# Performance work log

Measured on AMD Instinct MI355X. Metric: run time of the kernel, lower is better.

## Reference

```python
import jax, jax.numpy as jnp
import numpy as np

FS = 44100
LS = 1323000  # 30 s at 44.1 kHz (Ls/fs = 30 exactly)
FMIN, FMAX, BNDS = 32.7, 20000.0, 96
MIN_WIN = 4


def _design():
    """Reimplementation of LogScale + nsgfwin(sliced=False) + calcwinrange +
    the matrixform nsgtf loop parameters, producing a dense gather-index
    matrix idx [nbins, Mmax] and window matrix gw [nbins, Mmax]."""
    odiv = (np.log2(FMAX) - np.log2(FMIN)) / (BNDS - 1)
    pow2n = 2.0 ** odiv
    f = FMIN * pow2n ** np.arange(BNDS)
    lbas = BNDS
    frqs = np.concatenate(([0.0], f, [FS / 2.0]))
    fbas = np.concatenate((frqs, FS - frqs[-2:0:-1]))  # mirror negative freqs
    fbas *= float(LS) / FS
    # bandwidths M (window lengths)
    M = np.zeros(len(fbas), dtype=np.int64)
    M[0] = np.round(2 * fbas[1])
    for k in range(1, 2 * lbas + 1):
        M[k] = np.round(fbas[k + 1] - fbas[k - 1])
    M[-1] = np.round(LS - fbas[-2])
    M = np.maximum(M, MIN_WIN)
    # Hann windows (zero-frequency centered, hannwin)
    g = [0.5 * (np.cos(np.arange(m) * (2.0 * np.pi / m)) + 1.0) for m in M]
    # center positions rfbas (calcwinrange -> timepos == rfbas, nn == Ls)
    fb = fbas.copy()
    fb[lbas] = (fbas[lbas - 1] + fbas[lbas + 1]) / 2
    fb[lbas + 2] = LS - fb[lbas]
    rfbas = np.round(fb).astype(np.int64)
    nbins = len(g) // 2 + 1        # real=True, reducedform=0
    Mmax = int(M[:nbins].max())    # matrixform: all bins padded to Mmax
    idx = np.zeros((nbins, Mmax), dtype=np.int32)
    gw = np.zeros((nbins, Mmax), dtype=np.float32)
    for j in range(nbins):
        gj = g[j]
        Lg = len(gj)
        win = (np.arange(-(Lg // 2), Lg - (Lg // 2)) + rfbas[j]) % LS
        gs = np.fft.fftshift(gj)  # g is real -> conj is a no-op
        h1, h2 = (Lg + 1) // 2, Lg // 2
        # nsgtf placement: temp[:h1] = t[h2:], temp[-h2:] = t[:h2]
        idx[j, :h1] = win[h2:]
        gw[j, :h1] = gs[h2:]
        if h2 > 0:
            idx[j, Mmax - h2:] = win[:h2]
            gw[j, Mmax - h2:] = gs[:h2]
    return idx, gw


def setup_inputs() -> dict:
    key = jax.random.key(0)
    idx, gw = _design()
    s = jax.random.normal(key, (2, LS), dtype=jnp.float32)  # [channels, Ls]
    return {"s": s, "idx": jnp.asarray(idx), "gw": jnp.asarray(gw)}


def reference(s, idx, gw):
    # NSGT forward (nsgtf, matrixform, real): FFT the signal, gather each
    # frequency bin's circular window range, multiply by the fftshifted
    # window, zero-pad into a length-Mmax buffer, and IFFT per bin.
    ft = jnp.fft.fft(s.astype(jnp.complex64))          # [B, Ls]
    t = ft[:, idx] * gw                                # [B, nbins, Mmax]
    c = jnp.fft.ifft(t, axis=-1)                       # complex coefficients
    # pack complex output as trailing (real, imag) float32 channel
    return jnp.stack((c.real, c.imag), axis=-1)        # [B, nbins, Mmax, 2]
```

## Files before the change

### kernel.cpp

```cpp
#include <hip/hip_runtime.h>

#define LS 1323000
#define NB 98
#define MM 123000
#define N2 3000
#define BATCH 2
#define NROWS_T (NB*BATCH)
#define TWO_PI 6.28318530717958647692f

#define KBN 188
#define QN  96
#define SROW (KBN*QN*16)
#define QP  104

#define TBL2_OFF 0
#define TBL3_OFF 20
#define TBL4_OFF 120
#define TBL5_OFF 370
#define TBL_N    2995

typedef __attribute__((ext_vector_type(8))) short short8;
typedef __attribute__((ext_vector_type(4))) float f32x4;

__device__ __forceinline__ float2 cmul(float2 a, float2 b){
  return make_float2(a.x*b.x - a.y*b.y, a.x*b.y + a.y*b.x);
}
__device__ __forceinline__ unsigned short f2bf(float f){
  unsigned int u = __float_as_uint(f);
  unsigned int r = (u + 0x7FFFu + ((u >> 16) & 1u)) >> 16;
  return (unsigned short)r;
}

template<int R,int S>
__device__ __forceinline__ void butterfly(float2* v){
  if constexpr (R==4){
    float2 t0=make_float2(v[0].x+v[2].x, v[0].y+v[2].y);
    float2 t1=make_float2(v[0].x-v[2].x, v[0].y-v[2].y);
    float2 t2=make_float2(v[1].x+v[3].x, v[1].y+v[3].y);
    float2 t3=make_float2(v[1].x-v[3].x, v[1].y-v[3].y);
    v[0]=make_float2(t0.x+t2.x, t0.y+t2.y);
    v[2]=make_float2(t0.x-t2.x, t0.y-t2.y);
    v[1]=make_float2(t1.x - (float)S*t3.y, t1.y + (float)S*t3.x);
    v[3]=make_float2(t1.x + (float)S*t3.y, t1.y - (float)S*t3.x);
  } else if constexpr (R==8){
    float2 e[4]={v[0],v[2],v[4],v[6]};
    float2 o[4]={v[1],v[3],v[5],v[7]};
    butterfly<4,S>(e);
    butterfly<4,S>(o);
    const float h = 0.70710678118654752440f;
    float2 w1=make_float2(h, (float)S*h);
    float2 w2=make_float2(0.f, (float)S);
    float2 w3=make_float2(-h, (float)S*h);
    float2 o1=cmul(o[1],w1), o2=cmul(o[2],w2), o3=cmul(o[3],w3);
    v[0]=make_float2(e[0].x+o[0].x, e[0].y+o[0].y);
    v[4]=make_float2(e[0].x-o[0].x, e[0].y-o[0].y);
    v[1]=make_float2(e[1].x+o1.x, e[1].y+o1.y);
    v[5]=make_float2(e[1].x-o1.x, e[1].y-o1.y);
    v[2]=make_float2(e[2].x+o2.x, e[2].y+o2.y);
    v[6]=make_float2(e[2].x-o2.x, e[2].y-o2.y);
    v[3]=make_float2(e[3].x+o3.x, e[3].y+o3.y);
    v[7]=make_float2(e[3].x-o3.x, e[3].y-o3.y);
  } else {
    float2 x[R];
    #pragma unroll
    for(int k=0;k<R;k++){
      float2 acc=v[0];
      #pragma unroll
      for(int n=1;n<R;n++){
        const int p=(k*n)%R;
        float ang = (float)S * (TWO_PI/(float)R) * (float)p;
        float sn,cs; __sincosf(ang,&sn,&cs);
        acc.x += v[n].x*cs - v[n].y*sn;
        acc.y += v[n].x*sn + v[n].y*cs;
      }
      x[k]=acc;
    }
    #pragma unroll
    for(int k=0;k<R;k++) v[k]=x[k];
  }
}

template<int R,int S>
__global__ void __launch_bounds__(256)
fft_pass(const float2* __restrict__ in, float2* __restrict__ out,
         int N, int Ns){
  const int T = N / R;
  int j = blockIdx.x*blockDim.x + threadIdx.x;
  if (j >= T) return;
  int t = j % Ns;
  float u = (float)t / (float)(Ns*R);
  float ang = (float)S * TWO_PI * u;
  float sn,cs; __sincosf(ang,&sn,&cs);
  float2 w1=make_float2(cs,sn);
  float2 wr=make_float2(1.f,0.f);
  float2 v[R];
  #pragma unroll
  for(int r=0;r<R;r++){
    float2 a = in[j + r*T];
    v[r] = cmul(a, wr);
    wr = cmul(wr, w1);
  }
  butterfly<R,S>(v);
  int d = (j/Ns)*(Ns*R) + t;
  #pragma unroll
  for(int r=0;r<R;r++) out[d + r*Ns] = v[r];
}

__global__ void __launch_bounds__(256)
fft_c2c8(const float* __restrict__ s, float2* __restrict__ y){
  const int T = LS/8;
  int j = blockIdx.x*blockDim.x + threadIdx.x;
  if (j >= T) return;
  const float* x0 = s;
  const float* x1 = s + LS;
  float2 v[8];
  #pragma unroll
  for(int r=0;r<8;r++) v[r] = make_float2(x0[j + r*T], x1[j + r*T]);
  butterfly<8,-1>(v);
  int d = 8*j;
  #pragma unroll
  for(int r=0;r<8;r++) y[d + r] = v[r];
}

__global__ void span_init(int* __restrict__ spanA, int* __restrict__ spanB){
  int j = blockIdx.x*blockDim.x + threadIdx.x;
  if (j < NB){ spanA[j] = 0; spanB[j] = MM; }
}

#define SPAN_SLICE 4096
__global__ void __launch_bounds__(256)
rowspan_par(const float* __restrict__ gw, int* __restrict__ spanA,
            int* __restrict__ spanB){
  const int j  = blockIdx.x;
  const int lo = blockIdx.y * SPAN_SLICE;
  const int end = min(lo + SPAN_SLICE, MM);
  const float* g = gw + (size_t)j*MM;
  const int tid = threadIdx.x;
  int mA = -1, mB = MM;
  for (int m = lo + tid*4; m < end; m += 256*4){
    float4 v = *(const float4*)(g + m);
    #pragma unroll
    for (int t = 0; t < 4; t++){
      float f = ((const float*)&v)[t];
      int m2 = m + t;
      if (f != 0.f){
        if (m2 < 61500){ if (m2 > mA) mA = m2; }
        else           { if (m2 < mB) mB = m2; }
      }
    }
  }
  __shared__ int sA[256], sB[256];
  sA[tid]=mA; sB[tid]=mB; __syncthreads();
  for (int s=128; s>0; s>>=1){
    if (tid<s){ sA[tid]=max(sA[tid],sA[tid+s]); sB[tid]=min(sB[tid],sB[tid+s]); }
    __syncthreads();
  }
  if (tid==0){
    if (sA[0] >= 0) atomicMax(&spanA[j], sA[0]+1);
    if (sB[0] < MM) atomicMin(&spanB[j], sB[0]);
  }
}

__global__ void __launch_bounds__(256)
a_prep(unsigned short* __restrict__ A96){
  int i = blockIdx.x*blockDim.x + threadIdx.x;
  if (i >= 96*QP) return;
  int R = i / QP, q = i - R*QP;
  float val = 0.f;
  if (R < 82 && q < 82){
    int k2 = R >> 1, c = R & 1, n2 = q >> 1, cp = q & 1;
    int p = (k2*n2) % 41;
    float ang = (float)p * (TWO_PI/41.f);
    float sn, cs; sincosf(ang, &sn, &cs);
    val = c ? (cp ? cs : sn) : (cp ? -sn : cs);
  }
  A96[i] = f2bf(val);
}

__global__ void __launch_bounds__(256)
twid_prep(float2* __restrict__ tbl){
  int i = blockIdx.x*blockDim.x + threadIdx.x;
  if (i >= TBL_N) return;
  int t, r, den;
  if (i < TBL3_OFF)      { int l=i;          t=l/4; r=l%4+1; den=25;   }
  else if (i < TBL4_OFF) { int l=i-TBL3_OFF; t=l/4; r=l%4+1; den=125;  }
  else if (i < TBL5_OFF) { int l=i-TBL4_OFF; t=l/2; r=l%2+1; den=375;  }
  else                   { int l=i-TBL5_OFF; t=l/7; r=l%7+1; den=3000; }
  float ang = TWO_PI * (float)(t*r) / (float)den;
  float sn, cs; sincosf(ang, &sn, &cs);
  tbl[i] = make_float2(cs, sn);
}

#define PTILE 1681
__global__ void __launch_bounds__(256)
pack_gather(const float2* __restrict__ ft, const int* __restrict__ idx,
            const float* __restrict__ gw, const int* __restrict__ spanA,
            const int* __restrict__ spanB, float2* __restrict__ T, int row0){
  const int row  = row0 + blockIdx.y;
  const int jrow = row % NB;
  const int b    = row / NB;
  const int spA = spanA[jrow], spB = spanB[jrow];
  const int base = blockIdx.x * PTILE;
  const int end  = min(base + PTILE, MM);
  if (!(base < spA || end > spB)) return;
  __shared__ float2 tile[PTILE];
  const int cnt = end - base;
  const int*   idxr = idx + (size_t)jrow*MM;
  const float* gwr  = gw  + (size_t)jrow*MM;
  for (int l = threadIdx.x; l < cnt; l += 256){
    int n = base + l;
    float g = gwr[n] * (1.0f/(float)MM);
    int id = idxr[n];
    float2 F1 = ft[id];
    float2 F2 = ft[id ? (LS - id) : 0];
    float2 f;
    if (b == 0) f = make_float2(0.5f*(F1.x + F2.x), 0.5f*(F1.y - F2.y));
    else        f = make_float2(0.5f*(F1.y + F2.y), 0.5f*(F2.x - F1.x));
    tile[l] = make_float2(f.x*g, f.y*g);
  }
  __syncthreads();
  float2* Trow = T + (size_t)blockIdx.y*MM;
  const int bm = base % 41;
  for (int l2 = threadIdx.x; l2 < PTILE; l2 += 256){
    int n2 = l2 / 41, w = l2 - 41*n2;
    int l0 = n2 - bm; if (l0 < 0) l0 += 41;
    int l = l0 + 41*w;
    if (l < cnt){
      int n = base + l;
      if (n < spA || n >= spB){
        int ig = n / 41;
        Trow[(size_t)n2*N2 + ig] = tile[l];
      }
    }
  }
}

template<int R>
__device__ __forceinline__ void lds_stage1(const float2* src, float2* dst, int tid){
  const int T = N2 / R;
  for (int j = tid; j < T; j += 256){
    float2 v[R];
    #pragma unroll
    for (int r = 0; r < R; r++) v[r] = src[j + r*T];
    butterfly<R,1>(v);
    int d = j*R;
    #pragma unroll
    for (int r = 0; r < R; r++) dst[d + r] = v[r];
  }
}

template<int R, int Ns>
__device__ __forceinline__ void lds_stage_t(const float2* src, float2* dst,
                                            int tid, const float2* tw){
  const int T = N2 / R;
  for (int j = tid; j < T; j += 256){
    int t = j % Ns;
    const float2* w = tw + t*(R-1);
    float2 v[R];
    v[0] = src[j];
    #pragma unroll
    for (int r = 1; r < R; r++) v[r] = cmul(src[j + r*T], w[r-1]);
    butterfly<R,1>(v);
    int d = (j/Ns)*(Ns*R) + t;
    #pragma unroll
    for (int r = 0; r < R; r++) dst[d + r*Ns] = v[r];
  }
}

__global__ void __launch_bounds__(256)
inv_s1(const float2* __restrict__ T, const int* __restrict__ spanA,
       const int* __restrict__ spanB, const float2* __restrict__ tbl,
       unsigned short* __restrict__ Bb, int row0){
  __shared__ float2 u0[N2];
  __shared__ float2 u1[N2];
  __shared__ float2 tlds[TBL5_OFF];
  const int n2  = blockIdx.x;
  const int jrow = (row0 + blockIdx.y) % NB;
  const int tid = threadIdx.x;
  const int spA = spanA[jrow], spB = spanB[jrow];
  const int n1A = (spA - n2 + 40) / 41;
  const int n1B = (spB - n2 + 40) / 41;
  const float2* Trow = T + (size_t)blockIdx.y*MM + (size_t)n2*N2;
  for (int i = tid; i < N2; i += 256){
    float2 val = make_float2(0.f, 0.f);
    if (i < n1A || i >= n1B) val = Trow[i];
    u0[i] = val;
  }
  for (int i = tid; i < TBL5_OFF; i += 256) tlds[i] = tbl[i];
  __syncthreads();
  lds_stage1<5>(u0, u1, tid);                          __syncthreads();
  lds_stage_t<5,5>  (u1, u0, tid, tlds + TBL2_OFF);    __syncthreads();
  lds_stage_t<5,25> (u0, u1, tid, tlds + TBL3_OFF);    __syncthreads();
  lds_stage_t<3,125>(u1, u0, tid, tlds + TBL4_OFF);    __syncthreads();

  unsigned short* Brow = Bb + (size_t)blockIdx.y*SROW;
  const float2* tbl5 = tbl + TBL5_OFF;
  const int qr = 2*n2, qi = 2*n2+1;
  float sn, cs;
  __sincosf((float)(n2*375) * (TWO_PI/(float)MM), &sn, &cs);
  const float2 wstep = make_float2(cs, sn);
  for (int j = tid; j < 375; j += 256){
    const float2* w = tbl5 + j*7;
    float2 v[8];
    v[0] = u0[j];
    #pragma unroll
    for (int r = 1; r < 8; r++) v[r] = cmul(u0[j + r*375], w[r-1]);
    butterfly<8,1>(v);
    float ang = (float)(n2*j) * (TWO_PI/(float)MM);
    __sincosf(ang, &sn, &cs);
    float2 wf = make_float2(cs, sn);
    #pragma unroll
    for (int r = 0; r < 8; r++){
      float2 o = cmul(v[r], wf);
      int k1 = j + 375*r;
      int kb = k1 >> 4, kl = k1 & 15;
      size_t base = (size_t)kb*(QN*16) + kl;
      Brow[base + qr*16] = f2bf(o.x);
      Brow[base + qi*16] = f2bf(o.y);
      wf = cmul(wf, wstep);
    }
  }
}

__global__ void __launch_bounds__(256)
inv_s2_mfma(const unsigned short* __restrict__ A96,
            const unsigned short* __restrict__ Bb,
            float2* __restrict__ out){
  __shared__ unsigned short Als[96*QP];
  __shared__ unsigned short Bls[64*QP];
  const int tid = threadIdx.x;

  {
    const uint4* src = (const uint4*)A96;
    uint4* dst = (uint4*)Als;
    for (int f = tid; f < (96*QP*2)/16; f += 256) dst[f] = src[f];
  }
  {
    const unsigned short* Bt = Bb + (size_t)blockIdx.y*SROW
                                  + (size_t)blockIdx.x*4*(QN*16);
    for (int f = tid; f < 768; f += 256){
      uint4 d = *(const uint4*)(Bt + (size_t)f*8);
      int q   = (f >> 1) % QN;
      int kb  = f / (QN*2);
      int kl0 = (f & 1) * 8;
      if (q >= 82) d = make_uint4(0u,0u,0u,0u);
      const unsigned short* e = (const unsigned short*)&d;
      int rbase = kb*16 + kl0;
      #pragma unroll
      for (int j = 0; j < 8; j++)
        Bls[(rbase + j)*QP + q] = e[j];
    }
  }
  __syncthreads();

  const int w = tid >> 6, l = tid & 63;
  const int g = l >> 4, c = l & 15;

  f32x4 acc[6];
  #pragma unroll
  for (int m = 0; m < 6; m++) acc[m] = (f32x4){0.f,0.f,0.f,0.f};

  short8 b0 = *(const short8*)&Bls[(16*w + c)*QP +  0 + 8*g];
  short8 b1 = *(const short8*)&Bls[(16*w + c)*QP + 32 + 8*g];
  short8 b2 = *(const short8*)&Bls[(16*w + c)*QP + 64 + 8*g];
  #pragma unroll
  for (int m = 0; m < 6; m++){
    short8 a0 = *(const short8*)&Als[(16*m + c)*QP +  0 + 8*g];
    short8 a1 = *(const short8*)&Als[(16*m + c)*QP + 32 + 8*g];
    short8 a2 = *(const short8*)&Als[(16*m + c)*QP + 64 + 8*g];
    acc[m] = __builtin_amdgcn_mfma_f32_16x16x32_bf16(a0, b0, acc[m], 0, 0, 0);
    acc[m] = __builtin_amdgcn_mfma_f32_16x16x32_bf16(a1, b1, acc[m], 0, 0, 0);
    acc[m] = __builtin_amdgcn_mfma_f32_16x16x32_bf16(a2, b2, acc[m], 0, 0, 0);
  }

  float2* orow = out + (size_t)blockIdx.y*MM;
  int k1 = blockIdx.x*64 + 16*w + c;
  if (k1 < N2){
    #pragma unroll
    for (int m = 0; m < 6; m++){
      int R0 = 16*m + 4*g;
      int k2a = R0 >> 1;
      int k2b = k2a + 1;
      if (k2a < 41) orow[(size_t)k2a*N2 + k1] = make_float2(acc[m][0], acc[m][1]);
      if (k2b < 41) orow[(size_t)k2b*N2 + k1] = make_float2(acc[m][2], acc[m][3]);
    }
  }
}

extern "C" void kernel_launch(void* const* d_in, const int* in_sizes, int n_in,
                              void* d_out, int out_size, void* d_ws, size_t ws_size,
                              hipStream_t stream){
  const float* s   = (const float*)d_in[0];
  const int*   idx = (const int*)d_in[1];
  const float* gw  = (const float*)d_in[2];
  float2* out = (float2*)d_out;
  char* ws = (char*)d_ws;

  const size_t FWD_BYTES = 10584064;
  float2* bufA = (float2*)ws;
  float2* bufB = (float2*)(ws + FWD_BYTES);
  int* spanA = (int*)(ws + 2*FWD_BYTES);
  int* spanB = (int*)(ws + 2*FWD_BYTES + 512);
  unsigned short* A96 = (unsigned short*)(ws + 2*FWD_BYTES + 1024);
  const size_t A_BYTES = 20480;
  float2* tbl = (float2*)(ws + 2*FWD_BYTES + 1024 + A_BYTES);
  const size_t TBL_BYTES = 24576;
  unsigned short* Bbase = (unsigned short*)(ws + 2*FWD_BYTES + 1024 + A_BYTES + TBL_BYTES);

  a_prep<<<(96*QP + 255)/256, 256, 0, stream>>>(A96);
  twid_prep<<<(TBL_N + 255)/256, 256, 0, stream>>>(tbl);
  span_init<<<1, 128, 0, stream>>>(spanA, spanB);
  {
    dim3 g(NB, (MM + SPAN_SLICE - 1)/SPAN_SLICE);
    rowspan_par<<<g, 256, 0, stream>>>(gw, spanA, spanB);
  }

  {
    int blks = (LS/8 + 255)/256;
    fft_c2c8<<<blks,256,0,stream>>>(s, bufA);
  }
  float2* cur = bufA; float2* nxt = bufB;
  int Ns = 8;
  #define FWD(R) do{                                                         \
    int blks = (LS/(R) + 255)/256;                                           \
    fft_pass<R,-1><<<blks,256,0,stream>>>(cur, nxt, LS, Ns);                 \
    Ns *= (R);                                                               \
    { float2* tmp=cur; cur=nxt; nxt=tmp; }                                   \
  }while(0)
  FWD(7); FWD(7); FWD(5); FWD(5); FWD(5); FWD(3); FWD(3); FWD(3);
  #undef FWD

  const size_t row_bytes = (size_t)SROW * 2;
  size_t used = 2*FWD_BYTES + 1024 + A_BYTES + TBL_BYTES;
  size_t avail = (ws_size > used) ? (ws_size - used) : 0;
  int max_chunk = (int)(avail / row_bytes);
  if (max_chunk > NROWS_T) max_chunk = NROWS_T;
  if (max_chunk < 1) max_chunk = 1;

  const int ptiles = (MM + PTILE - 1)/PTILE;
  for (int c0 = 0; c0 < NROWS_T; c0 += max_chunk){
    int cr = NROWS_T - c0; if (cr > max_chunk) cr = max_chunk;
    float2* Tchunk = out + (size_t)c0*MM;
    dim3 g0(ptiles, cr);
    pack_gather<<<g0,256,0,stream>>>(cur, idx, gw, spanA, spanB, Tchunk, c0);
    dim3 g1(41, cr);
    inv_s1<<<g1,256,0,stream>>>(Tchunk, spanA, spanB, tbl, Bbase, c0);
    dim3 g2(47, cr);
    inv_s2_mfma<<<g2,256,0,stream>>>(A96, Bbase, Tchunk);
  }
}
```

Before: 515.0 us.

## Use radix-15 forward FFT passes and widen inverse stage-one blocks

Replaces the six radix-5/radix-3 forward FFT passes with three radix-15 passes built from a 3x5 prime-factor butterfly. This cuts the number of full-signal global memory round trips in the forward transform. Also raises the inv_s1 block size to 512 threads and pads the twiddle tables to 5/3 strides. The cost is more registers per radix-15 thread and different occupancy in inv_s1.

```diff
diff --git a/kernel.cpp b/kernel.cpp
--- a/kernel.cpp
+++ b/kernel.cpp
@@ -13,11 +13,13 @@
 #define SROW (KBN*QN*16)
 #define QP  104
 
-#define TBL2_OFF 0
-#define TBL3_OFF 20
-#define TBL4_OFF 120
-#define TBL5_OFF 370
-#define TBL_N    2995
+#define P2 0
+#define P3 25
+#define P4 150
+#define P5 525
+#define TBL_N 3150
+
+#define NT1 512
 
 typedef __attribute__((ext_vector_type(8))) short short8;
 typedef __attribute__((ext_vector_type(4))) float f32x4;
@@ -60,6 +62,39 @@
     v[6]=make_float2(e[2].x-o2.x, e[2].y-o2.y);
     v[3]=make_float2(e[3].x+o3.x, e[3].y+o3.y);
     v[7]=make_float2(e[3].x-o3.x, e[3].y-o3.y);
+  } else if constexpr (R==15){
+    float2 A[5][3];
+    #pragma unroll
+    for (int b=0;b<5;b++){
+      float2 t[3] = { v[b], v[b+5], v[b+10] };
+      butterfly<3,S>(t);
+      #pragma unroll
+      for (int m=0;m<3;m++) A[b][m]=t[m];
+    }
+    constexpr float CC[5][3] = {
+      {1.f, 1.f, 1.f},
+      {1.f,  0.91354545764260090f,  0.66913060635885820f},
+      {1.f,  0.66913060635885820f, -0.10452846326765346f},
+      {1.f,  0.30901699437494745f, -0.80901699437494745f},
+      {1.f, -0.10452846326765346f, -0.97814760073380570f}};
+    constexpr float SS[5][3] = {
+      {0.f, 0.f, 0.f},
+      {0.f, 0.40673664307580015f, 0.74314482547739420f},
+      {0.f, 0.74314482547739420f, 0.99452189536827330f},
+      {0.f, 0.95105651629515350f, 0.58778525229247310f},
+      {0.f, 0.99452189536827330f, -0.20791169081775931f}};
+    #pragma unroll
+    for (int m=0;m<3;m++){
+      float2 t5[5];
+      #pragma unroll
+      for (int b=0;b<5;b++){
+        float2 w = make_float2(CC[b][m], (float)S*SS[b][m]);
+        t5[b] = cmul(A[b][m], w);
+      }
+      butterfly<5,S>(t5);
+      #pragma unroll
+      for (int c=0;c<5;c++) v[m+3*c]=t5[c];
+    }
   } else {
     float2 x[R];
     #pragma unroll
@@ -181,14 +216,18 @@
 twid_prep(float2* __restrict__ tbl){
   int i = blockIdx.x*blockDim.x + threadIdx.x;
   if (i >= TBL_N) return;
-  int t, r, den;
-  if (i < TBL3_OFF)      { int l=i;          t=l/4; r=l%4+1; den=25;   }
-  else if (i < TBL4_OFF) { int l=i-TBL3_OFF; t=l/4; r=l%4+1; den=125;  }
-  else if (i < TBL5_OFF) { int l=i-TBL4_OFF; t=l/2; r=l%2+1; den=375;  }
-  else                   { int l=i-TBL5_OFF; t=l/7; r=l%7+1; den=3000; }
-  float ang = TWO_PI * (float)(t*r) / (float)den;
-  float sn, cs; sincosf(ang, &sn, &cs);
-  tbl[i] = make_float2(cs, sn);
+  int t=0, r=0, den=1; bool valid=true;
+  if (i < P3)      { t=i/5;          int rm=i%5;        valid=(rm<4); r=rm+1; den=25;   }
+  else if (i < P4) { int l=i-P3; t=l/5; int rm=l%5;     valid=(rm<4); r=rm+1; den=125;  }
+  else if (i < P5) { int l=i-P4; t=l/3; int rm=l%3;     valid=(rm<2); r=rm+1; den=375;  }
+  else             { int l=i-P5; t=l/7; r=l%7+1;        den=3000; }
+  float2 w = make_float2(1.f, 0.f);
+  if (valid){
+    float ang = TWO_PI * (float)(t*r) / (float)den;
+    float sn, cs; sincosf(ang, &sn, &cs);
+    w = make_float2(cs, sn);
+  }
+  tbl[i] = w;
 }
 
 #define PTILE 1681
@@ -235,10 +274,10 @@
   }
 }
 
-template<int R>
+template<int R, int NT>
 __device__ __forceinline__ void lds_stage1(const float2* src, float2* dst, int tid){
   const int T = N2 / R;
-  for (int j = tid; j < T; j += 256){
+  for (int j = tid; j < T; j += NT){
     float2 v[R];
     #pragma unroll
     for (int r = 0; r < R; r++) v[r] = src[j + r*T];
@@ -249,13 +288,13 @@
   }
 }
 
-template<int R, int Ns>
+template<int R, int Ns, int TS, int NT>
 __device__ __forceinline__ void lds_stage_t(const float2* src, float2* dst,
                                             int tid, const float2* tw){
   const int T = N2 / R;
-  for (int j = tid; j < T; j += 256){
+  for (int j = tid; j < T; j += NT){
     int t = j % Ns;
-    const float2* w = tw + t*(R-1);
+    const float2* w = tw + t*TS;
     float2 v[R];
     v[0] = src[j];
     #pragma unroll
@@ -267,13 +306,13 @@
   }
 }
 
-__global__ void __launch_bounds__(256)
+__global__ void __launch_bounds__(NT1)
 inv_s1(const float2* __restrict__ T, const int* __restrict__ spanA,
        const int* __restrict__ spanB, const float2* __restrict__ tbl,
        unsigned short* __restrict__ Bb, int row0){
   __shared__ float2 u0[N2];
   __shared__ float2 u1[N2];
-  __shared__ float2 tlds[TBL5_OFF];
+  __shared__ float2 tlds[P5];
   const int n2  = blockIdx.x;
   const int jrow = (row0 + blockIdx.y) % NB;
   const int tid = threadIdx.x;
@@ -281,25 +320,25 @@
   const int n1A = (spA - n2 + 40) / 41;
   const int n1B = (spB - n2 + 40) / 41;
   const float2* Trow = T + (size_t)blockIdx.y*MM + (size_t)n2*N2;
-  for (int i = tid; i < N2; i += 256){
+  for (int i = tid; i < N2; i += NT1){
     float2 val = make_float2(0.f, 0.f);
     if (i < n1A || i >= n1B) val = Trow[i];
     u0[i] = val;
   }
-  for (int i = tid; i < TBL5_OFF; i += 256) tlds[i] = tbl[i];
+  for (int i = tid; i < P5; i += NT1) tlds[i] = tbl[i];
   __syncthreads();
-  lds_stage1<5>(u0, u1, tid);                          __syncthreads();
-  lds_stage_t<5,5>  (u1, u0, tid, tlds + TBL2_OFF);    __syncthreads();
-  lds_stage_t<5,25> (u0, u1, tid, tlds + TBL3_OFF);    __syncthreads();
-  lds_stage_t<3,125>(u1, u0, tid, tlds + TBL4_OFF);    __syncthreads();
+  lds_stage1<5,NT1>(u0, u1, tid);                       __syncthreads();
+  lds_stage_t<5,5,5,NT1>  (u1, u0, tid, tlds + P2);     __syncthreads();
+  lds_stage_t<5,25,5,NT1> (u0, u1, tid, tlds + P3);     __syncthreads();
+  lds_stage_t<3,125,3,NT1>(u1, u0, tid, tlds + P4);     __syncthreads();
 
   unsigned short* Brow = Bb + (size_t)blockIdx.y*SROW;
-  const float2* tbl5 = tbl + TBL5_OFF;
+  const float2* tbl5 = tbl + P5;
   const int qr = 2*n2, qi = 2*n2+1;
   float sn, cs;
   __sincosf((float)(n2*375) * (TWO_PI/(float)MM), &sn, &cs);
   const float2 wstep = make_float2(cs, sn);
-  for (int j = tid; j < 375; j += 256){
+  for (int j = tid; j < 375; j += NT1){
     const float2* w = tbl5 + j*7;
     float2 v[8];
     v[0] = u0[j];
@@ -404,7 +443,7 @@
   unsigned short* A96 = (unsigned short*)(ws + 2*FWD_BYTES + 1024);
   const size_t A_BYTES = 20480;
   float2* tbl = (float2*)(ws + 2*FWD_BYTES + 1024 + A_BYTES);
-  const size_t TBL_BYTES = 24576;
+  const size_t TBL_BYTES = 25600;
   unsigned short* Bbase = (unsigned short*)(ws + 2*FWD_BYTES + 1024 + A_BYTES + TBL_BYTES);
 
   a_prep<<<(96*QP + 255)/256, 256, 0, stream>>>(A96);
@@ -427,7 +466,7 @@
     Ns *= (R);                                                               \
     { float2* tmp=cur; cur=nxt; nxt=tmp; }                                   \
   }while(0)
-  FWD(7); FWD(7); FWD(5); FWD(5); FWD(5); FWD(3); FWD(3); FWD(3);
+  FWD(7); FWD(7); FWD(15); FWD(15); FWD(15);
   #undef FWD
 
   const size_t row_bytes = (size_t)SROW * 2;
@@ -444,7 +483,7 @@
     dim3 g0(ptiles, cr);
     pack_gather<<<g0,256,0,stream>>>(cur, idx, gw, spanA, spanB, Tchunk, c0);
     dim3 g1(41, cr);
-    inv_s1<<<g1,256,0,stream>>>(Tchunk, spanA, spanB, tbl, Bbase, c0);
+    inv_s1<<<g1,NT1,0,stream>>>(Tchunk, spanA, spanB, tbl, Bbase, c0);
     dim3 g2(47, cr);
     inv_s2_mfma<<<g2,256,0,stream>>>(A96, Bbase, Tchunk);
   }
```

Result: faster. 478.1 us (-7.2%).
